# Kernel optimization log

Measured on AMD Instinct MI355X. Metric: run time of the kernel, lower is better.

Reference implementation:

```python
import jax, jax.numpy as jnp
import numpy as np


def setup_inputs() -> dict:
    key = jax.random.key(0)
    ks = jax.random.split(key, 7)
    B, C, T = 64, 2048, 256  # T must equal C // heads (see module's matmul(attn, v))
    s = 0.02
    return {
        "x": jax.random.normal(ks[0], (B, C, T), dtype=jnp.float32),
        "Wq": jax.random.normal(ks[1], (C, C), dtype=jnp.float32) * s,
        "bq": jax.random.normal(ks[2], (C,), dtype=jnp.float32) * s,
        "Wk": jax.random.normal(ks[3], (C, C), dtype=jnp.float32) * s,
        "bk": jax.random.normal(ks[4], (C,), dtype=jnp.float32) * s,
        "Wv": jax.random.normal(ks[5], (C, C), dtype=jnp.float32) * s,
        "bv": jax.random.normal(ks[6], (C,), dtype=jnp.float32) * s,
        "heads": 8,
    }


def reference(x, Wq, bq, Wk, bk, Wv, bv, heads):
    B, C, T = x.shape
    H = heads
    D = C // H  # must equal T for this module's math
    scale = float(D) ** -0.5

    def proj(W, b):
        # 1x1 Conv1d == per-timestep linear: out[b,o,t] = sum_c W[o,c] x[b,c,t] + b[o]
        return jnp.einsum('oc,bct->bot', W, x) + b[None, :, None]

    q = proj(Wq, bq).reshape(B, H, D, T).transpose(0, 1, 3, 2)  # (B,H,T,D)
    k = proj(Wk, bk).reshape(B, H, D, T).transpose(0, 1, 3, 2)  # (B,H,T,D)
    v = proj(Wv, bv).reshape(B, H, D, T)                         # (B,H,D,T), D==T

    attn = jax.nn.softmax(jnp.einsum('bhid,bhjd->bhij', q, k) * scale, axis=-1)  # (B,H,T,T)
    # Faithful to torch: matmul(attn, v) with v UNpermuted -> contract attn's last axis with v's D axis
    out = jnp.einsum('bhik,bhkj->bhij', attn, v)  # (B,H,T,T)
    return out.reshape(B, C, T)
```

## Files before the change

### kernel.cpp

```cpp
#include <hip/hip_runtime.h>


typedef __attribute__((ext_vector_type(8))) short    bf16x8;
typedef __attribute__((ext_vector_type(4))) float    f32x4;
typedef __attribute__((ext_vector_type(4))) unsigned short us4;
typedef __attribute__((ext_vector_type(8))) unsigned short us8;
typedef unsigned short u16;
typedef unsigned int   u32;

#define CC 2048
#define TT 256
#define BB 64
#define HH 8
#define DD 256

__device__ __forceinline__ u16 f2bf(float f) {
  u32 u = __builtin_bit_cast(u32, f);
  u32 r = (u + 0x7fffu + ((u >> 16) & 1u)) >> 16;
  return (u16)r;
}
__device__ __forceinline__ float bf2f(u16 b) {
  u32 u = ((u32)b) << 16;
  return __builtin_bit_cast(float, u);
}

__device__ __forceinline__ void async16(const void* g, void* l) {
  __builtin_amdgcn_global_load_lds(
      (const __attribute__((address_space(1))) u32*)g,
      (__attribute__((address_space(3))) u32*)l, 16, 0, 0);
}

__global__ __launch_bounds__(256) void wconv_kernel(
    const float* __restrict__ w0, const float* __restrict__ w1,
    const float* __restrict__ w2, u16* __restrict__ dst) {
  int p = blockIdx.y;
  const float* s = (p == 0) ? w0 : (p == 1) ? w1 : w2;
  size_t i = ((size_t)blockIdx.x * 256 + threadIdx.x) * 4;
  float4 v = *(const float4*)(s + i);
  us4 o = {f2bf(v.x), f2bf(v.y), f2bf(v.z), f2bf(v.w)};
  *(us4*)(dst + (size_t)p * CC * CC + i) = o;
}

__global__ __launch_bounds__(256) void xt_kernel(
    const float* __restrict__ x, u16* __restrict__ xT) {
  __shared__ float tile[64][68];
  int t0 = blockIdx.x * 64;
  int c0 = blockIdx.y * 64;
  int b  = blockIdx.z;
  int tid = threadIdx.x;
  int lr = tid >> 4;
  int lc = (tid & 15) * 4;
  const float* src = x + ((size_t)b * CC + c0) * TT + t0;
#pragma unroll
  for (int s = 0; s < 4; ++s) {
    int c = s * 16 + lr;
    float4 v = *(const float4*)(src + (size_t)c * TT + lc);
    *(float4*)&tile[c][lc] = v;
  }
  __syncthreads();
  int t  = tid >> 2;
  int cb = (tid & 3) * 16;
  u16 tmp[16];
#pragma unroll
  for (int e = 0; e < 16; ++e) tmp[e] = f2bf(tile[cb + e][t]);
  u16* dst = xT + ((size_t)b * TT + t0 + t) * CC + c0 + cb;
  *(us8*)dst       = *(const us8*)&tmp[0];
  *(us8*)(dst + 8) = *(const us8*)&tmp[8];
}

__global__ __launch_bounds__(512, 2) void proj_kernel(
    const u16* __restrict__ Wbf, const u16* __restrict__ xT,
    const float* __restrict__ bq, const float* __restrict__ bk,
    const float* __restrict__ bv, u16* __restrict__ qkv) {
  __shared__ __align__(16) u16 As[2][16384];
  __shared__ __align__(16) u16 Bs[2][16384];

  int tid = threadIdx.x;
  int bid = blockIdx.x;
  int wg  = (bid & 7) * 192 + (bid >> 3);
  int pm  = wg >> 6;
  int b   = wg & 63;
  int proj = pm >> 3;
  int mt   = pm & 7;
  int m0   = mt << 8;

  const u16* Ap = Wbf + (size_t)proj * CC * CC + (size_t)m0 * CC;
  const u16* Xp = xT + (size_t)b * TT * CC;
  const float* bias = (proj == 0) ? bq : (proj == 1) ? bk : bv;

  int lane = tid & 63, w = tid >> 6;
  int wm = w >> 2, wn = w & 3;
  int ar = lane & 15, kq = lane >> 4;

  int r_b = tid >> 3;
  int c8  = tid & 7;
  int c8s = c8 ^ (r_b & 7);
  const size_t go = (size_t)r_b * CC + (size_t)c8s * 8;
  const int ldsq = r_b * 64 + c8 * 8;

  const int cx = (kq ^ (ar & 7)) * 8;

  const int arow = wm * 16 + ar;
  const int brow = wn * 16 + ar;

#define STG_A(buf, kt, h)                                                     \
  do {                                                                        \
    async16(Ap + (size_t)((h) * 128) * CC + (size_t)(kt) * 64 + go,           \
            &As[buf][(h) * 8192 + ldsq]);                                     \
    async16(Ap + (size_t)((h) * 128 + 64) * CC + (size_t)(kt) * 64 + go,      \
            &As[buf][(h) * 8192 + 4096 + ldsq]);                              \
  } while (0)
#define STG_B(buf, kt, h)                                                     \
  do {                                                                        \
    async16(Xp + (size_t)((h) * 128) * CC + (size_t)(kt) * 64 + go,           \
            &Bs[buf][(h) * 8192 + ldsq]);                                     \
    async16(Xp + (size_t)((h) * 128 + 64) * CC + (size_t)(kt) * 64 + go,      \
            &Bs[buf][(h) * 8192 + 4096 + ldsq]);                              \
  } while (0)

  bf16x8 af[4][2], bfr[2][2];
  f32x4 acc[8][4] = {};

#define LDA(buf, mh)                                                          \
  do {                                                                        \
    _Pragma("unroll") for (int fl = 0; fl < 4; ++fl) {                        \
      int row = ((mh) * 4 + fl) * 32 + arow;                                  \
      af[fl][0] = *(const bf16x8*)&As[buf][row * 64 + cx];                    \
      af[fl][1] = *(const bf16x8*)&As[buf][row * 64 + (cx ^ 32)];             \
    }                                                                         \
  } while (0)
#define LDB(buf, nh)                                                          \
  do {                                                                        \
    _Pragma("unroll") for (int gl = 0; gl < 2; ++gl) {                        \
      int row = ((nh) * 2 + gl) * 64 + brow;                                  \
      bfr[gl][0] = *(const bf16x8*)&Bs[buf][row * 64 + cx];                   \
      bfr[gl][1] = *(const bf16x8*)&Bs[buf][row * 64 + (cx ^ 32)];            \
    }                                                                         \
  } while (0)
#define MMA(mh, nh)                                                           \
  do {                                                                        \
    _Pragma("unroll") for (int fl = 0; fl < 4; ++fl) {                        \
      _Pragma("unroll") for (int gl = 0; gl < 2; ++gl) {                      \
        acc[(mh) * 4 + fl][(nh) * 2 + gl] =                                   \
            __builtin_amdgcn_mfma_f32_16x16x32_bf16(                          \
                af[fl][0], bfr[gl][0], acc[(mh) * 4 + fl][(nh) * 2 + gl], 0,  \
                0, 0);                                                        \
        acc[(mh) * 4 + fl][(nh) * 2 + gl] =                                   \
            __builtin_amdgcn_mfma_f32_16x16x32_bf16(                          \
                af[fl][1], bfr[gl][1], acc[(mh) * 4 + fl][(nh) * 2 + gl], 0,  \
                0, 0);                                                        \
      }                                                                       \
    }                                                                         \
  } while (0)
#define PRE(buf, mh, nh)                                                      \
  do {                                                                        \
    if ((nh) == 0) LDA(buf, mh);                                              \
    LDB(buf, nh);                                                             \
  } while (0)
#define POST(mh, nh)                                                          \
  do {                                                                        \
    __builtin_amdgcn_s_barrier();                                             \
    asm volatile("s_waitcnt lgkmcnt(0)" ::: "memory");                        \
    __builtin_amdgcn_sched_barrier(0);                                        \
    __builtin_amdgcn_s_setprio(1);                                            \
    MMA(mh, nh);                                                              \
    __builtin_amdgcn_s_setprio(0);                                            \
    __builtin_amdgcn_sched_barrier(0);                                        \
    __builtin_amdgcn_s_barrier();                                             \
  } while (0)
#define VM4 asm volatile("s_waitcnt vmcnt(4)" ::: "memory")
#define VM0 asm volatile("s_waitcnt vmcnt(0)" ::: "memory")

  STG_A(0, 0, 0); STG_B(0, 0, 0); STG_A(0, 0, 1); STG_B(0, 0, 1);
  STG_A(1, 1, 0); STG_B(1, 1, 0);
  VM4;
  __builtin_amdgcn_s_barrier();

  for (int i = 0; i < 15; ++i) {
    int k = 2 * i;
    PRE(0, 0, 0); STG_A(1, k + 1, 1);      POST(0, 0);
    PRE(0, 0, 1); STG_B(1, k + 1, 1);      POST(0, 1);
    PRE(0, 1, 0); STG_A(0, k + 2, 0);      POST(1, 0);
    PRE(0, 1, 1); STG_B(0, k + 2, 0); VM4; POST(1, 1);
    PRE(1, 0, 0); STG_A(0, k + 2, 1);      POST(0, 0);
    PRE(1, 0, 1); STG_B(0, k + 2, 1);      POST(0, 1);
    PRE(1, 1, 0); STG_A(1, k + 3, 0);      POST(1, 0);
    PRE(1, 1, 1); STG_B(1, k + 3, 0); VM4; POST(1, 1);
  }
  PRE(0, 0, 0); STG_A(1, 31, 1);           POST(0, 0);
  PRE(0, 0, 1); STG_B(1, 31, 1);           POST(0, 1);
  PRE(0, 1, 0);                            POST(1, 0);
  PRE(0, 1, 1);                       VM0; POST(1, 1);
  PRE(1, 0, 0);                            POST(0, 0);
  PRE(1, 0, 1);                            POST(0, 1);
  PRE(1, 1, 0);                            POST(1, 0);
  PRE(1, 1, 1);                            POST(1, 1);

  u16* outp = qkv + (size_t)proj * BB * CC * TT +
              (size_t)(b * HH + mt) * TT * DD;
#pragma unroll
  for (int f = 0; f < 8; ++f) {
    int d0 = f * 32 + wm * 16 + kq * 4;
    float b0 = bias[m0 + d0],     b1 = bias[m0 + d0 + 1];
    float b2 = bias[m0 + d0 + 2], b3 = bias[m0 + d0 + 3];
#pragma unroll
    for (int g = 0; g < 4; ++g) {
      int t = g * 64 + wn * 16 + ar;
      f32x4 v = acc[f][g];
      us4 pk = {f2bf(v[0] + b0), f2bf(v[1] + b1), f2bf(v[2] + b2),
                f2bf(v[3] + b3)};
      *(us4*)(outp + (size_t)t * DD + d0) = pk;
    }
  }
#undef STG_A
#undef STG_B
#undef LDA
#undef LDB
#undef MMA
#undef PRE
#undef POST
#undef VM4
#undef VM0
}

__global__ __launch_bounds__(256) void attn_kernel(
    const u16* __restrict__ qkv, float* __restrict__ out) {
  __shared__ __align__(16) u16 As[64 * 32];
  __shared__ __align__(16) u16 Bs[256 * 32];
  __shared__ __align__(16) u16 Ps[64 * 264];
  __shared__ float rowpart[64][4];
  __shared__ float inv[64];

  int tid = threadIdx.x;
  int i0 = blockIdx.x * 64;
  int bh = blockIdx.y;
  const size_t hd = (size_t)TT * DD;
  const u16* Q = qkv + (size_t)bh * hd;
  const u16* K = qkv + (size_t)(BB * HH + bh) * hd;
  const u16* V = qkv + (size_t)(2 * BB * HH + bh) * hd;

  int lane = tid & 63, w = tid >> 6;
  int ar = lane & 15, kq = lane >> 4;
  int arow = tid >> 2, acol = (tid & 3) * 8;

  const u16* Qbase = Q + (size_t)(i0 + arow) * DD + acol;
  const u16* Kbase = K + (size_t)arow * DD + acol;
  const u16* Vbase = V + (size_t)arow * DD + acol;

  f32x4 acc[4][4] = {};
  for (int k0 = 0; k0 < DD; k0 += 32) {
    async16(Qbase + k0, As + tid * 8);
#pragma unroll
    for (int s = 0; s < 4; ++s)
      async16(Kbase + (size_t)(s * 64) * DD + k0, Bs + s * 2048 + tid * 8);
    __syncthreads();
    bf16x8 af[4], bfv[4];
#pragma unroll
    for (int mt = 0; mt < 4; ++mt)
      af[mt] = *(const bf16x8*)&As[(mt * 16 + ar) * 32 + kq * 8];
#pragma unroll
    for (int nt = 0; nt < 4; ++nt)
      bfv[nt] = *(const bf16x8*)&Bs[(w * 64 + nt * 16 + ar) * 32 + kq * 8];
#pragma unroll
    for (int mt = 0; mt < 4; ++mt)
#pragma unroll
      for (int nt = 0; nt < 4; ++nt)
        acc[mt][nt] = __builtin_amdgcn_mfma_f32_16x16x32_bf16(
            af[mt], bfv[nt], acc[mt][nt], 0, 0, 0);
    __syncthreads();
  }
  const float scale = 0.0625f;
#pragma unroll
  for (int mt = 0; mt < 4; ++mt) {
    float ps[4] = {0.f, 0.f, 0.f, 0.f};
#pragma unroll
    for (int nt = 0; nt < 4; ++nt) {
      f32x4 v = acc[mt][nt];
#pragma unroll
      for (int r = 0; r < 4; ++r) {
        float p = __expf(v[r] * scale);
        u16 pb = f2bf(p);
        Ps[(mt * 16 + kq * 4 + r) * 264 + (w * 64 + nt * 16 + ar)] = pb;
        ps[r] += bf2f(pb);
      }
    }
#pragma unroll
    for (int r = 0; r < 4; ++r) {
      float s = ps[r];
      s += __shfl_xor(s, 1, 64);
      s += __shfl_xor(s, 2, 64);
      s += __shfl_xor(s, 4, 64);
      s += __shfl_xor(s, 8, 64);
      if (ar == 0) rowpart[mt * 16 + kq * 4 + r][w] = s;
    }
  }
  __syncthreads();
  if (tid < 64) {
    float s = rowpart[tid][0] + rowpart[tid][1] + rowpart[tid][2] +
              rowpart[tid][3];
    inv[tid] = 1.0f / s;
  }
#pragma unroll
  for (int mt = 0; mt < 4; ++mt)
#pragma unroll
    for (int nt = 0; nt < 4; ++nt) acc[mt][nt] = (f32x4){0.f, 0.f, 0.f, 0.f};
  for (int k0 = 0; k0 < TT; k0 += 32) {
#pragma unroll
    for (int s = 0; s < 4; ++s)
      async16(Vbase + (size_t)(s * 64) * DD + k0, Bs + s * 2048 + tid * 8);
    __syncthreads();
    bf16x8 af[4], bfv[4];
#pragma unroll
    for (int mt = 0; mt < 4; ++mt)
      af[mt] = *(const bf16x8*)&Ps[(mt * 16 + ar) * 264 + k0 + kq * 8];
#pragma unroll
    for (int nt = 0; nt < 4; ++nt)
      bfv[nt] = *(const bf16x8*)&Bs[(w * 64 + nt * 16 + ar) * 32 + kq * 8];
#pragma unroll
    for (int mt = 0; mt < 4; ++mt)
#pragma unroll
      for (int nt = 0; nt < 4; ++nt)
        acc[mt][nt] = __builtin_amdgcn_mfma_f32_16x16x32_bf16(
            af[mt], bfv[nt], acc[mt][nt], 0, 0, 0);
    __syncthreads();
  }
  int b = bh >> 3, h = bh & 7;
  float* obase = out + ((size_t)b * CC + h * TT + i0) * TT;
#pragma unroll
  for (int mt = 0; mt < 4; ++mt)
#pragma unroll
    for (int r = 0; r < 4; ++r) {
      int m = mt * 16 + kq * 4 + r;
      float iv = inv[m];
#pragma unroll
      for (int nt = 0; nt < 4; ++nt) {
        int n = w * 64 + nt * 16 + ar;
        obase[(size_t)m * TT + n] = acc[mt][nt][r] * iv;
      }
    }
}

extern "C" void kernel_launch(void* const* d_in, const int* in_sizes, int n_in,
                              void* d_out, int out_size, void* d_ws,
                              size_t ws_size, hipStream_t stream) {
  const float* x  = (const float*)d_in[0];
  const float* Wq = (const float*)d_in[1];
  const float* bq = (const float*)d_in[2];
  const float* Wk = (const float*)d_in[3];
  const float* bk = (const float*)d_in[4];
  const float* Wv = (const float*)d_in[5];
  const float* bv = (const float*)d_in[6];
  float* out = (float*)d_out;

  char* ws = (char*)d_ws;
  u16* xT  = (u16*)ws;
  u16* Wbf = (u16*)(ws + 67108864);
  u16* qkv = (u16*)(ws + 67108864 + 25165824);

  wconv_kernel<<<dim3(4096, 3, 1), 256, 0, stream>>>(Wq, Wk, Wv, Wbf);
  xt_kernel<<<dim3(4, 32, 64), 256, 0, stream>>>(x, xT);
  proj_kernel<<<dim3(1536, 1, 1), 512, 0, stream>>>(Wbf, xT, bq, bk, bv, qkv);
  attn_kernel<<<dim3(4, 512, 1), 256, 0, stream>>>(qkv, out);
}
```

Baseline: 852.6 us.

## Load all B fragments once per k-tile and halve barrier phases in QKV GEMM

The QKV projection main loop now reads all four B fragments from LDS once per k-tile instead of reloading half of them for each of the two M halves. The software pipeline is collapsed from eight barrier-delimited phases per two k-tiles to four, with global-to-LDS staging regrouped to match. The goal is fewer redundant LDS reads and fewer workgroup barriers. The cost is eight more bf16x8 registers held live, which could raise register pressure. There is also less interleaving between LDS loads and MFMA issue.

```diff
diff --git a/kernel.cpp b/kernel.cpp
--- a/kernel.cpp
+++ b/kernel.cpp
@@ -118,7 +118,7 @@
             &Bs[buf][(h) * 8192 + 4096 + ldsq]);                              \
   } while (0)
 
-  bf16x8 af[4][2], bfr[2][2];
+  bf16x8 af[4][2], bfr[4][2];
   f32x4 acc[8][4] = {};
 
 #define LDA(buf, mh)                                                          \
@@ -129,41 +129,32 @@
       af[fl][1] = *(const bf16x8*)&As[buf][row * 64 + (cx ^ 32)];             \
     }                                                                         \
   } while (0)
-#define LDB(buf, nh)                                                          \
-  do {                                                                        \
-    _Pragma("unroll") for (int gl = 0; gl < 2; ++gl) {                        \
-      int row = ((nh) * 2 + gl) * 64 + brow;                                  \
-      bfr[gl][0] = *(const bf16x8*)&Bs[buf][row * 64 + cx];                   \
-      bfr[gl][1] = *(const bf16x8*)&Bs[buf][row * 64 + (cx ^ 32)];            \
+#define LDBALL(buf)                                                           \
+  do {                                                                        \
+    _Pragma("unroll") for (int g = 0; g < 4; ++g) {                           \
+      int row = g * 64 + brow;                                                \
+      bfr[g][0] = *(const bf16x8*)&Bs[buf][row * 64 + cx];                    \
+      bfr[g][1] = *(const bf16x8*)&Bs[buf][row * 64 + (cx ^ 32)];             \
     }                                                                         \
   } while (0)
-#define MMA(mh, nh)                                                           \
+#define MMA_MH(mh)                                                            \
   do {                                                                        \
     _Pragma("unroll") for (int fl = 0; fl < 4; ++fl) {                        \
-      _Pragma("unroll") for (int gl = 0; gl < 2; ++gl) {                      \
-        acc[(mh) * 4 + fl][(nh) * 2 + gl] =                                   \
-            __builtin_amdgcn_mfma_f32_16x16x32_bf16(                          \
-                af[fl][0], bfr[gl][0], acc[(mh) * 4 + fl][(nh) * 2 + gl], 0,  \
-                0, 0);                                                        \
-        acc[(mh) * 4 + fl][(nh) * 2 + gl] =                                   \
-            __builtin_amdgcn_mfma_f32_16x16x32_bf16(                          \
-                af[fl][1], bfr[gl][1], acc[(mh) * 4 + fl][(nh) * 2 + gl], 0,  \
-                0, 0);                                                        \
+      _Pragma("unroll") for (int g = 0; g < 4; ++g) {                         \
+        acc[(mh) * 4 + fl][g] = __builtin_amdgcn_mfma_f32_16x16x32_bf16(      \
+            af[fl][0], bfr[g][0], acc[(mh) * 4 + fl][g], 0, 0, 0);            \
+        acc[(mh) * 4 + fl][g] = __builtin_amdgcn_mfma_f32_16x16x32_bf16(      \
+            af[fl][1], bfr[g][1], acc[(mh) * 4 + fl][g], 0, 0, 0);            \
       }                                                                       \
     }                                                                         \
   } while (0)
-#define PRE(buf, mh, nh)                                                      \
-  do {                                                                        \
-    if ((nh) == 0) LDA(buf, mh);                                              \
-    LDB(buf, nh);                                                             \
-  } while (0)
-#define POST(mh, nh)                                                          \
+#define POSTF(mh)                                                             \
   do {                                                                        \
     __builtin_amdgcn_s_barrier();                                             \
     asm volatile("s_waitcnt lgkmcnt(0)" ::: "memory");                        \
     __builtin_amdgcn_sched_barrier(0);                                        \
     __builtin_amdgcn_s_setprio(1);                                            \
-    MMA(mh, nh);                                                              \
+    MMA_MH(mh);                                                               \
     __builtin_amdgcn_s_setprio(0);                                            \
     __builtin_amdgcn_sched_barrier(0);                                        \
     __builtin_amdgcn_s_barrier();                                             \
@@ -178,23 +169,31 @@
 
   for (int i = 0; i < 15; ++i) {
     int k = 2 * i;
-    PRE(0, 0, 0); STG_A(1, k + 1, 1);      POST(0, 0);
-    PRE(0, 0, 1); STG_B(1, k + 1, 1);      POST(0, 1);
-    PRE(0, 1, 0); STG_A(0, k + 2, 0);      POST(1, 0);
-    PRE(0, 1, 1); STG_B(0, k + 2, 0); VM4; POST(1, 1);
-    PRE(1, 0, 0); STG_A(0, k + 2, 1);      POST(0, 0);
-    PRE(1, 0, 1); STG_B(0, k + 2, 1);      POST(0, 1);
-    PRE(1, 1, 0); STG_A(1, k + 3, 0);      POST(1, 0);
-    PRE(1, 1, 1); STG_B(1, k + 3, 0); VM4; POST(1, 1);
-  }
-  PRE(0, 0, 0); STG_A(1, 31, 1);           POST(0, 0);
-  PRE(0, 0, 1); STG_B(1, 31, 1);           POST(0, 1);
-  PRE(0, 1, 0);                            POST(1, 0);
-  PRE(0, 1, 1);                       VM0; POST(1, 1);
-  PRE(1, 0, 0);                            POST(0, 0);
-  PRE(1, 0, 1);                            POST(0, 1);
-  PRE(1, 1, 0);                            POST(1, 0);
-  PRE(1, 1, 1);                            POST(1, 1);
+    LDA(0, 0); LDBALL(0);
+    STG_B(1, k + 1, 1); STG_A(1, k + 1, 1);
+    POSTF(0);
+    LDA(0, 1);
+    STG_A(0, k + 2, 0); STG_B(0, k + 2, 0);
+    VM4;
+    POSTF(1);
+    LDA(1, 0); LDBALL(1);
+    STG_B(0, k + 2, 1); STG_A(0, k + 2, 1);
+    POSTF(0);
+    LDA(1, 1);
+    STG_A(1, k + 3, 0); STG_B(1, k + 3, 0);
+    VM4;
+    POSTF(1);
+  }
+  LDA(0, 0); LDBALL(0);
+  STG_B(1, 31, 1); STG_A(1, 31, 1);
+  POSTF(0);
+  LDA(0, 1);
+  VM0;
+  POSTF(1);
+  LDA(1, 0); LDBALL(1);
+  POSTF(0);
+  LDA(1, 1);
+  POSTF(1);
 
   u16* outp = qkv + (size_t)proj * BB * CC * TT +
               (size_t)(b * HH + mt) * TT * DD;
@@ -215,10 +214,9 @@
 #undef STG_A
 #undef STG_B
 #undef LDA
-#undef LDB
-#undef MMA
-#undef PRE
-#undef POST
+#undef LDBALL
+#undef MMA_MH
+#undef POSTF
 #undef VM4
 #undef VM0
 }
```

Result: faster. 814.7 us (-4.4%).
